# Kernel optimization log

Hardware: AMD Instinct MI355X
Metric: run time of the kernel (lower is better)

## Reference

```python
import jax, jax.numpy as jnp
import numpy as np

B, N, M = 4, 8192, 8192


def setup_inputs() -> dict:
    key = jax.random.key(0)
    k1, k2, k3, k4 = jax.random.split(key, 4)
    xyz1 = jax.random.normal(k1, (B, N, 3), dtype=jnp.float32)
    xyz2 = jax.random.normal(k2, (B, M, 3), dtype=jnp.float32)
    weights1 = jax.random.uniform(k3, (B, N), dtype=jnp.float32)
    weights2 = jax.random.uniform(k4, (B, M), dtype=jnp.float32)
    return {"xyz1": xyz1, "xyz2": xyz2, "weights1": weights1, "weights2": weights2}


def _chamfer_dists(xyz1, xyz2):
    # Squared L2 pairwise distances via the ||a||^2 + ||b||^2 - 2 a.b identity
    # (avoids materializing a [B, N, M, 3] difference tensor).
    sq1 = jnp.sum(xyz1 * xyz1, axis=-1)            # [B, N]
    sq2 = jnp.sum(xyz2 * xyz2, axis=-1)            # [B, M]
    dots = jnp.einsum("bnc,bmc->bnm", xyz1, xyz2)  # [B, N, M]
    d = sq1[:, :, None] + sq2[:, None, :] - 2.0 * dots
    d = jnp.maximum(d, 0.0)
    dist1 = jnp.min(d, axis=2)  # [B, N] nearest in xyz2 for each point in xyz1
    dist2 = jnp.min(d, axis=1)  # [B, M] nearest in xyz1 for each point in xyz2
    return dist1, dist2


def reference(xyz1, xyz2, weights1, weights2):
    dist1, dist2 = _chamfer_dists(xyz1, xyz2)
    dist1 = dist1 * weights1
    dist2 = dist2 * weights2
    dist1_avg = jnp.sum(dist1) / jnp.sum(weights1)
    dist2_avg = jnp.sum(dist2) / jnp.sum(weights2)
    return (dist1_avg + dist2_avg) / 2.0
```

## Files before the change

### kernel.cpp

```cpp
#include <hip/hip_runtime.h>

#define TPB 256
#define TPBM 512
constexpr int Bsz  = 4;
constexpr int Npts = 8192;
constexpr int Mpts = 8192;
constexpr int PTS  = Bsz * Npts;
constexpr int QT_PER_B = Npts / 32;
constexpr int CT_PER_B = Mpts / 32;
constexpr int RBLK = 64;

typedef __attribute__((ext_vector_type(8)))  short short8;
typedef __attribute__((ext_vector_type(16))) float f32x16;

__device__ __forceinline__ float min3f(float a, float b, float c) {
    return fminf(fminf(a, b), c);
}

__device__ __forceinline__ f32x16 mfma_32x32(short8 a, short8 b) {
    f32x16 d;
    asm("v_mfma_f32_32x32x16_bf16 %0, %1, %2, 0\n\t"
        "s_nop 7\n\t"
        "s_nop 7\n\t"
        "s_nop 3"
        : "=&v"(d) : "v"(a), "v"(b));
    return d;
}

__device__ __forceinline__ unsigned short bfh(float v) {
    unsigned u = __float_as_uint(v);
    return (unsigned short)((u + 0x7fffu + ((u >> 16) & 1u)) >> 16);
}
__device__ __forceinline__ float b2f(unsigned short h) {
    return __uint_as_float(((unsigned)h) << 16);
}
__device__ __forceinline__ void split2(float v, unsigned short& h,
                                       unsigned short& m) {
    h = bfh(v); m = bfh(v - b2f(h));
}
__device__ __forceinline__ void split3(float v, unsigned short& h,
                                       unsigned short& m, unsigned short& l) {
    h = bfh(v); float fh = b2f(h);
    m = bfh(v - fh); float fm = b2f(m);
    l = bfh(v - fh - fm);
}

__global__ void __launch_bounds__(TPB) prep_kernel(
    const float* __restrict__ xyz1, const float* __restrict__ xyz2,
    short* __restrict__ aQ, short* __restrict__ bC)
{
    int id   = blockIdx.x * TPB + threadIdx.x;
    int side = id >> 16;
    int tl   = id & 65535;
    int tile = tl >> 6, lane = tl & 63;
    int r = lane & 31, g = lane >> 5;

    const float* src = side ? xyz2 : xyz1;
    int p = tile * 32 + r;
    float x = src[p * 3 + 0], y = src[p * 3 + 1], z = src[p * 3 + 2];
    float n = fmaf(x, x, fmaf(y, y, z * z));
    float s = side ? 1.f : -2.f;

    unsigned short xh, xm, yh, ym, zh, zm, nh, nm, nl;
    split2(s * x, xh, xm);
    split2(s * y, yh, ym);
    split2(s * z, zh, zm);
    split3(n, nh, nm, nl);
    const unsigned short ONE = 0x3F80;

    short8 v;
#pragma unroll
    for (int j = 0; j < 8; ++j) {
        int k = g * 8 + j;
        unsigned short u = 0;
        if (k < 9) {
            int c = k / 3, o = k - 3 * c;
            unsigned short h = c == 0 ? xh : (c == 1 ? yh : zh);
            unsigned short m = c == 0 ? xm : (c == 1 ? ym : zm);
            u = side ? (o == 1 ? m : h)
                     : (o < 2 ? h : m);
        } else if (k < 12) {
            u = side ? ONE : (k == 9 ? nh : (k == 10 ? nm : nl));
        } else if (k < 15) {
            u = side ? (k == 12 ? nh : (k == 13 ? nm : nl)) : ONE;
        }
        v[j] = (short)u;
    }
    short8* dst = (short8*)(side ? bC : aQ);
    dst[tile * 64 + lane] = v;
}

__global__ void __launch_bounds__(TPBM, 8) chamfer_mfma_kernel(
    const short* __restrict__ aQ, const short* __restrict__ bC,
    unsigned int* __restrict__ partials)
{
    int bid = blockIdx.x;
    int linear = (bid & 7) * 128 + (bid >> 3);
    int batch = linear >> 8;
    int rem = linear & 255;
    int qs = rem >> 3;
    int cs = rem & 7;
    int w = threadIdx.x >> 6, lane = threadIdx.x & 63;

    int qtile  = batch * QT_PER_B + qs * 8 + w;
    int ctile0 = batch * CT_PER_B + cs * 32;

    const short8* aT = (const short8*)aQ;
    const short8* bT = (const short8*)bC;

    __shared__ unsigned int colb[1024];
    colb[threadIdx.x]       = 0x7f7fffffu;
    colb[threadIdx.x + 512] = 0x7f7fffffu;

    short8 a = aT[qtile * 64 + lane];

    f32x16 rowp;
#pragma unroll
    for (int i = 0; i < 16; ++i) rowp[i] = 3.4e38f;
    __syncthreads();

    const short8* bP = bT + ctile0 * 64 + lane;
    unsigned int* mycol = &colb[lane & 31];

    short8 b0 = bP[0], b1;

#pragma unroll 2
    for (int ct = 0; ct < 32; ct += 2) {
        b1 = bP[(ct + 1) * 64];
        {
            f32x16 d = mfma_32x32(a, b0);
            rowp = __builtin_elementwise_min(rowp, d);
            float ca = min3f(d[0], d[1], d[2]);
            ca = min3f(ca, d[3], d[4]);
            ca = min3f(ca, d[5], d[6]);
            ca = fminf(ca, d[7]);
            float cb = min3f(d[8], d[9], d[10]);
            cb = min3f(cb, d[11], d[12]);
            cb = min3f(cb, d[13], d[14]);
            cb = fminf(cb, d[15]);
            atomicMin(mycol + ct * 32,
                      __float_as_uint(fmaxf(fminf(ca, cb), 0.f)));
        }
        b0 = bP[(ct + 2) * 64];
        {
            f32x16 d = mfma_32x32(a, b1);
            rowp = __builtin_elementwise_min(rowp, d);
            float ca = min3f(d[0], d[1], d[2]);
            ca = min3f(ca, d[3], d[4]);
            ca = min3f(ca, d[5], d[6]);
            ca = fminf(ca, d[7]);
            float cb = min3f(d[8], d[9], d[10]);
            cb = min3f(cb, d[11], d[12]);
            cb = min3f(cb, d[13], d[14]);
            cb = fminf(cb, d[15]);
            atomicMin(mycol + (ct + 1) * 32,
                      __float_as_uint(fmaxf(fminf(ca, cb), 0.f)));
        }
    }

#pragma unroll
    for (int i = 0; i < 16; ++i) {
        float v = rowp[i];
        v = fminf(v, __shfl_xor(v, 1));
        v = fminf(v, __shfl_xor(v, 2));
        v = fminf(v, __shfl_xor(v, 4));
        v = fminf(v, __shfl_xor(v, 8));
        v = fminf(v, __shfl_xor(v, 16));
        if ((lane & 31) == 0) {
            int row = (i & 3) + 4 * (lane >> 5) + 8 * (i >> 2);
            atomicMin(&partials[qtile * 32 + row],
                      __float_as_uint(fmaxf(v, 0.f)));
        }
    }

    __syncthreads();
    int cbase = PTS + ctile0 * 32;
    atomicMin(&partials[cbase + threadIdx.x],       colb[threadIdx.x]);
    atomicMin(&partials[cbase + threadIdx.x + 512], colb[threadIdx.x + 512]);
}

__global__ void __launch_bounds__(TPB) reduce_kernel(
    const float* __restrict__ partials,
    const float* __restrict__ w1, const float* __restrict__ w2,
    float2* __restrict__ slots)
{
    int gid = blockIdx.x * TPB + threadIdx.x;
    int dir = gid >> 13;
    int idx = gid & 8191;
    const float4* d4 = (const float4*)(partials + (size_t)dir * PTS);
    const float4* w4 = (const float4*)(dir ? w2 : w1);
    float4 d = d4[idx], w = w4[idx];
    float c = d.x * w.x + d.y * w.y + d.z * w.z + d.w * w.w;
    float s = w.x + w.y + w.z + w.w;

    for (int off = 32; off; off >>= 1) {
        c += __shfl_down(c, off);
        s += __shfl_down(s, off);
    }
    __shared__ float sc[4], ss[4];
    int lane = threadIdx.x & 63, wid = threadIdx.x >> 6;
    if (lane == 0) { sc[wid] = c; ss[wid] = s; }
    __syncthreads();
    if (threadIdx.x == 0) {
        slots[blockIdx.x] =
            make_float2(sc[0] + sc[1] + sc[2] + sc[3],
                        ss[0] + ss[1] + ss[2] + ss[3]);
    }
}

__global__ void __launch_bounds__(64) final_kernel(
    const float2* __restrict__ slots, float* __restrict__ out)
{
    float2 v = slots[threadIdx.x];
    for (int off = 16; off; off >>= 1) {
        v.x += __shfl_down(v.x, off, 32);
        v.y += __shfl_down(v.y, off, 32);
    }
    float c1 = __shfl(v.x, 32), s1 = __shfl(v.y, 32);
    if (threadIdx.x == 0)
        out[0] = 0.5f * (v.x / v.y + c1 / s1);
}

extern "C" void kernel_launch(void* const* d_in, const int* in_sizes, int n_in,
                              void* d_out, int out_size, void* d_ws, size_t ws_size,
                              hipStream_t stream) {
    const float* xyz1 = (const float*)d_in[0];
    const float* xyz2 = (const float*)d_in[1];
    const float* w1   = (const float*)d_in[2];
    const float* w2   = (const float*)d_in[3];
    float* out = (float*)d_out;

    unsigned int* partials = (unsigned int*)d_ws;
    float2* slots = (float2*)((char*)d_ws + (size_t)2 * PTS * sizeof(unsigned int));
    short* aQ = (short*)((char*)d_ws + (1u << 20));
    short* bC = (short*)((char*)d_ws + (4u << 20));

    prep_kernel<<<512, TPB, 0, stream>>>(xyz1, xyz2, aQ, bC);
    chamfer_mfma_kernel<<<1024, TPBM, 0, stream>>>(aQ, bC, partials);
    reduce_kernel<<<RBLK, TPB, 0, stream>>>((const float*)partials, w1, w2, slots);
    final_kernel<<<1, 64, 0, stream>>>(slots, out);
}
```

Baseline: 97.06 us.

## Fuse bf16 fragment packing into chamfer kernel and merge reduction kernels

Drops the separate prep kernel: each block now packs its candidate tiles from xyz2 into shared memory and its query fragment from xyz1 in registers, then runs the MFMA loop reading B fragments from LDS. The two reduction kernels become a single 1024-thread block that computes both weighted sums and the final ratio. This removes two kernel launches and the global round trip of the packed fragments. In exchange, packing is recomputed by every block (candidate tiles are repacked by 32 query-slice blocks each), and the added 32KB of LDS may lower occupancy. The single-block reduction also has far less parallelism than the previous 64-block version.

```diff
diff --git a/kernel.cpp b/kernel.cpp
--- a/kernel.cpp
+++ b/kernel.cpp
@@ -1,14 +1,13 @@
 #include <hip/hip_runtime.h>
 
-#define TPB 256
 #define TPBM 512
+#define TPBR 1024
 constexpr int Bsz  = 4;
 constexpr int Npts = 8192;
 constexpr int Mpts = 8192;
 constexpr int PTS  = Bsz * Npts;
 constexpr int QT_PER_B = Npts / 32;
 constexpr int CT_PER_B = Mpts / 32;
-constexpr int RBLK = 64;
 
 typedef __attribute__((ext_vector_type(8)))  short short8;
 typedef __attribute__((ext_vector_type(16))) float f32x16;
@@ -45,29 +44,16 @@
     l = bfh(v - fh - fm);
 }
 
-__global__ void __launch_bounds__(TPB) prep_kernel(
-    const float* __restrict__ xyz1, const float* __restrict__ xyz2,
-    short* __restrict__ aQ, short* __restrict__ bC)
-{
-    int id   = blockIdx.x * TPB + threadIdx.x;
-    int side = id >> 16;
-    int tl   = id & 65535;
-    int tile = tl >> 6, lane = tl & 63;
-    int r = lane & 31, g = lane >> 5;
-
-    const float* src = side ? xyz2 : xyz1;
-    int p = tile * 32 + r;
-    float x = src[p * 3 + 0], y = src[p * 3 + 1], z = src[p * 3 + 2];
+__device__ __forceinline__ short8 pack_frag(float x, float y, float z,
+                                            int side, int g) {
     float n = fmaf(x, x, fmaf(y, y, z * z));
     float s = side ? 1.f : -2.f;
-
     unsigned short xh, xm, yh, ym, zh, zm, nh, nm, nl;
     split2(s * x, xh, xm);
     split2(s * y, yh, ym);
     split2(s * z, zh, zm);
     split3(n, nh, nm, nl);
     const unsigned short ONE = 0x3F80;
-
     short8 v;
 #pragma unroll
     for (int j = 0; j < 8; ++j) {
@@ -86,12 +72,11 @@
         }
         v[j] = (short)u;
     }
-    short8* dst = (short8*)(side ? bC : aQ);
-    dst[tile * 64 + lane] = v;
-}
-
-__global__ void __launch_bounds__(TPBM, 8) chamfer_mfma_kernel(
-    const short* __restrict__ aQ, const short* __restrict__ bC,
+    return v;
+}
+
+__global__ void __launch_bounds__(TPBM, 8) chamfer_fused_kernel(
+    const float* __restrict__ xyz1, const float* __restrict__ xyz2,
     unsigned int* __restrict__ partials)
 {
     int bid = blockIdx.x;
@@ -100,62 +85,57 @@
     int rem = linear & 255;
     int qs = rem >> 3;
     int cs = rem & 7;
-    int w = threadIdx.x >> 6, lane = threadIdx.x & 63;
+    int tid = threadIdx.x;
+    int w = tid >> 6, lane = tid & 63;
 
     int qtile  = batch * QT_PER_B + qs * 8 + w;
     int ctile0 = batch * CT_PER_B + cs * 32;
 
-    const short8* aT = (const short8*)aQ;
-    const short8* bT = (const short8*)bC;
-
+    __shared__ short8 sc[2048];
     __shared__ unsigned int colb[1024];
-    colb[threadIdx.x]       = 0x7f7fffffu;
-    colb[threadIdx.x + 512] = 0x7f7fffffu;
-
-    short8 a = aT[qtile * 64 + lane];
+    colb[tid]       = 0x7f7fffffu;
+    colb[tid + 512] = 0x7f7fffffu;
+
+#pragma unroll
+    for (int i = 0; i < 4; ++i) {
+        int e = tid + i * 512;
+        int ct = e >> 6, ln = e & 63;
+        int p = (ctile0 + ct) * 32 + (ln & 31);
+        sc[e] = pack_frag(xyz2[p * 3 + 0], xyz2[p * 3 + 1], xyz2[p * 3 + 2],
+                          1, ln >> 5);
+    }
+
+    short8 a;
+    {
+        int p = qtile * 32 + (lane & 31);
+        a = pack_frag(xyz1[p * 3 + 0], xyz1[p * 3 + 1], xyz1[p * 3 + 2],
+                      0, lane >> 5);
+    }
 
     f32x16 rowp;
 #pragma unroll
     for (int i = 0; i < 16; ++i) rowp[i] = 3.4e38f;
     __syncthreads();
 
-    const short8* bP = bT + ctile0 * 64 + lane;
     unsigned int* mycol = &colb[lane & 31];
-
-    short8 b0 = bP[0], b1;
+    short8 b = sc[lane];
 
 #pragma unroll 2
-    for (int ct = 0; ct < 32; ct += 2) {
-        b1 = bP[(ct + 1) * 64];
-        {
-            f32x16 d = mfma_32x32(a, b0);
-            rowp = __builtin_elementwise_min(rowp, d);
-            float ca = min3f(d[0], d[1], d[2]);
-            ca = min3f(ca, d[3], d[4]);
-            ca = min3f(ca, d[5], d[6]);
-            ca = fminf(ca, d[7]);
-            float cb = min3f(d[8], d[9], d[10]);
-            cb = min3f(cb, d[11], d[12]);
-            cb = min3f(cb, d[13], d[14]);
-            cb = fminf(cb, d[15]);
-            atomicMin(mycol + ct * 32,
-                      __float_as_uint(fmaxf(fminf(ca, cb), 0.f)));
-        }
-        b0 = bP[(ct + 2) * 64];
-        {
-            f32x16 d = mfma_32x32(a, b1);
-            rowp = __builtin_elementwise_min(rowp, d);
-            float ca = min3f(d[0], d[1], d[2]);
-            ca = min3f(ca, d[3], d[4]);
-            ca = min3f(ca, d[5], d[6]);
-            ca = fminf(ca, d[7]);
-            float cb = min3f(d[8], d[9], d[10]);
-            cb = min3f(cb, d[11], d[12]);
-            cb = min3f(cb, d[13], d[14]);
-            cb = fminf(cb, d[15]);
-            atomicMin(mycol + (ct + 1) * 32,
-                      __float_as_uint(fmaxf(fminf(ca, cb), 0.f)));
-        }
+    for (int ct = 0; ct < 32; ++ct) {
+        short8 bn = sc[((ct + 1) & 31) * 64 + lane];
+        f32x16 d = mfma_32x32(a, b);
+        rowp = __builtin_elementwise_min(rowp, d);
+        float ca = min3f(d[0], d[1], d[2]);
+        ca = min3f(ca, d[3], d[4]);
+        ca = min3f(ca, d[5], d[6]);
+        ca = fminf(ca, d[7]);
+        float cb = min3f(d[8], d[9], d[10]);
+        cb = min3f(cb, d[11], d[12]);
+        cb = min3f(cb, d[13], d[14]);
+        cb = fminf(cb, d[15]);
+        atomicMin(mycol + ct * 32,
+                  __float_as_uint(fmaxf(fminf(ca, cb), 0.f)));
+        b = bn;
     }
 
 #pragma unroll
@@ -175,50 +155,54 @@
 
     __syncthreads();
     int cbase = PTS + ctile0 * 32;
-    atomicMin(&partials[cbase + threadIdx.x],       colb[threadIdx.x]);
-    atomicMin(&partials[cbase + threadIdx.x + 512], colb[threadIdx.x + 512]);
-}
-
-__global__ void __launch_bounds__(TPB) reduce_kernel(
+    atomicMin(&partials[cbase + tid],       colb[tid]);
+    atomicMin(&partials[cbase + tid + 512], colb[tid + 512]);
+}
+
+__global__ void __launch_bounds__(TPBR) reduce_final_kernel(
     const float* __restrict__ partials,
     const float* __restrict__ w1, const float* __restrict__ w2,
-    float2* __restrict__ slots)
+    float* __restrict__ out)
 {
-    int gid = blockIdx.x * TPB + threadIdx.x;
-    int dir = gid >> 13;
-    int idx = gid & 8191;
-    const float4* d4 = (const float4*)(partials + (size_t)dir * PTS);
-    const float4* w4 = (const float4*)(dir ? w2 : w1);
-    float4 d = d4[idx], w = w4[idx];
-    float c = d.x * w.x + d.y * w.y + d.z * w.z + d.w * w.w;
-    float s = w.x + w.y + w.z + w.w;
+    int tid = threadIdx.x;
+    const float4* d4 = (const float4*)partials;
+    const float4* w14 = (const float4*)w1;
+    const float4* w24 = (const float4*)w2;
+
+    float c0 = 0.f, s0 = 0.f, c1 = 0.f, s1 = 0.f;
+#pragma unroll
+    for (int i = 0; i < 8; ++i) {
+        int idx = tid + i * TPBR;
+        float4 d = d4[idx], w = w14[idx];
+        c0 += d.x * w.x + d.y * w.y + d.z * w.z + d.w * w.w;
+        s0 += w.x + w.y + w.z + w.w;
+    }
+#pragma unroll
+    for (int i = 0; i < 8; ++i) {
+        int idx = tid + i * TPBR;
+        float4 d = d4[8192 + idx], w = w24[idx];
+        c1 += d.x * w.x + d.y * w.y + d.z * w.z + d.w * w.w;
+        s1 += w.x + w.y + w.z + w.w;
+    }
 
     for (int off = 32; off; off >>= 1) {
-        c += __shfl_down(c, off);
-        s += __shfl_down(s, off);
-    }
-    __shared__ float sc[4], ss[4];
-    int lane = threadIdx.x & 63, wid = threadIdx.x >> 6;
-    if (lane == 0) { sc[wid] = c; ss[wid] = s; }
+        c0 += __shfl_down(c0, off); s0 += __shfl_down(s0, off);
+        c1 += __shfl_down(c1, off); s1 += __shfl_down(s1, off);
+    }
+    __shared__ float4 red[16];
+    int lane = tid & 63, wid = tid >> 6;
+    if (lane == 0) red[wid] = make_float4(c0, s0, c1, s1);
     __syncthreads();
-    if (threadIdx.x == 0) {
-        slots[blockIdx.x] =
-            make_float2(sc[0] + sc[1] + sc[2] + sc[3],
-                        ss[0] + ss[1] + ss[2] + ss[3]);
-    }
-}
-
-__global__ void __launch_bounds__(64) final_kernel(
-    const float2* __restrict__ slots, float* __restrict__ out)
-{
-    float2 v = slots[threadIdx.x];
-    for (int off = 16; off; off >>= 1) {
-        v.x += __shfl_down(v.x, off, 32);
-        v.y += __shfl_down(v.y, off, 32);
-    }
-    float c1 = __shfl(v.x, 32), s1 = __shfl(v.y, 32);
-    if (threadIdx.x == 0)
-        out[0] = 0.5f * (v.x / v.y + c1 / s1);
+    if (tid < 64) {
+        float4 v = tid < 16 ? red[tid] : make_float4(0.f, 0.f, 0.f, 0.f);
+        for (int off = 8; off; off >>= 1) {
+            v.x += __shfl_down(v.x, off, 16);
+            v.y += __shfl_down(v.y, off, 16);
+            v.z += __shfl_down(v.z, off, 16);
+            v.w += __shfl_down(v.w, off, 16);
+        }
+        if (tid == 0) out[0] = 0.5f * (v.x / v.y + v.z / v.w);
+    }
 }
 
 extern "C" void kernel_launch(void* const* d_in, const int* in_sizes, int n_in,
@@ -231,12 +215,8 @@
     float* out = (float*)d_out;
 
     unsigned int* partials = (unsigned int*)d_ws;
-    float2* slots = (float2*)((char*)d_ws + (size_t)2 * PTS * sizeof(unsigned int));
-    short* aQ = (short*)((char*)d_ws + (1u << 20));
-    short* bC = (short*)((char*)d_ws + (4u << 20));
-
-    prep_kernel<<<512, TPB, 0, stream>>>(xyz1, xyz2, aQ, bC);
-    chamfer_mfma_kernel<<<1024, TPBM, 0, stream>>>(aQ, bC, partials);
-    reduce_kernel<<<RBLK, TPB, 0, stream>>>((const float*)partials, w1, w2, slots);
-    final_kernel<<<1, 64, 0, stream>>>(slots, out);
-}
+
+    chamfer_fused_kernel<<<1024, TPBM, 0, stream>>>(xyz1, xyz2, partials);
+    reduce_final_kernel<<<1, TPBR, 0, stream>>>((const float*)partials,
+                                                w1, w2, out);
+}
```

Measured after the change: 92.48 us. 1.05x faster.
